# Performance work log

Measured on AMD Instinct MI355X. Metric: run time of the kernel, lower is better.

Reference implementation:

```python
import jax, jax.numpy as jnp
import numpy as np

B, C, L, D, H = 8, 64, 128, 768, 768  # batch, candidates, tokens, hidden, mlp hidden


def setup_inputs() -> dict:
    key = jax.random.key(0)
    k0, k1, k2 = jax.random.split(key, 3)
    inp = jax.random.normal(k0, (B, C, 2, L, D), dtype=jnp.float32)
    # MlpModule params (input_size = 768*2): Linear(2D->H) -> ReLU -> Linear(H->1)
    W1 = jax.random.normal(k1, (2 * D, H), dtype=jnp.float32) * 0.02
    b1 = jnp.zeros((H,), dtype=jnp.float32)
    W2 = jax.random.normal(k2, (H, 1), dtype=jnp.float32) * 0.02
    b2 = jnp.zeros((1,), dtype=jnp.float32)
    return {"input": inp, "W1": W1, "b1": b1, "W2": W2, "b2": b2}


def reference(input, W1, b1, W2, b2):
    b, c, _, l, d = input.shape
    context = input[:, :, 0].reshape(b * c, l, d)  # [BC, L, D]
    entity = input[:, :, 1].reshape(b * c, l, d)   # [BC, L, D]
    mask = (context[:, :, 0] != 0).astype(context.dtype)  # [BC, L]

    # bmm similarity: [BC, L, L]
    sim = jnp.einsum('bld,bmd->blm', context, entity)
    dot_scores = jnp.max(sim, axis=-1)          # [BC, L]
    argmax_values = jnp.argmax(sim, axis=-1)    # [BC, L]

    # gather best-matching entity token per context token: [BC, L, D]
    gathered = jnp.take_along_axis(entity, argmax_values[..., None], axis=1)

    # MLP over stacked (context, entity) pair -> flatten to 2D features
    mlp_in = jnp.concatenate([context, gathered], axis=-1)  # [BC, L, 2D]
    h = jax.nn.relu(mlp_in @ W1 + b1)
    scores = (h @ W2 + b2)[..., 0]              # [BC, L]

    scores = jnp.sum(scores * mask, axis=-1)              # [BC]
    dot_scores = jnp.sum(dot_scores * mask, axis=-1).reshape(b, c)  # [B, C]
    return scores, dot_scores
```

## Files before the change

### kernel.cpp

```cpp
#include <hip/hip_runtime.h>
#include <hip/hip_bf16.h>
#include <stdint.h>

#define NPAIR 512
#define LTOK  128
#define DDIM  768
#define HDIM  768
#define K2    1536
#define MARGIN 0.4f

typedef float f32x4 __attribute__((ext_vector_type(4)));
typedef short bf16x8 __attribute__((ext_vector_type(8)));

static __device__ __forceinline__ int fsw(int row) {
    return (row ^ (row >> 2)) & 3;
}

static __device__ __forceinline__ unsigned short f2bf(float f) {
    union { float f; uint32_t u; } v; v.f = f;
    uint32_t u = v.u;
    u += 0x7FFF + ((u >> 16) & 1);
    return (unsigned short)(u >> 16);
}

static __device__ __forceinline__ uint2 pack4(f32x4 v) {
    __hip_bfloat162 lo = __float22bfloat162_rn(float2{v[0], v[1]});
    __hip_bfloat162 hi = __float22bfloat162_rn(float2{v[2], v[3]});
    uint2 r;
    r.x = *reinterpret_cast<unsigned*>(&lo);
    r.y = *reinterpret_cast<unsigned*>(&hi);
    return r;
}

static __device__ __forceinline__ uint4 pack8(f32x4 a, f32x4 b) {
    uint2 lo = pack4(a), hi = pack4(b);
    uint4 r; r.x = lo.x; r.y = lo.y; r.z = hi.x; r.w = hi.y;
    return r;
}

typedef const __attribute__((address_space(1))) void* gas_t;
typedef __attribute__((address_space(3))) void* las_t;
static __device__ __forceinline__ void gld16(const void* g, void* l) {
    __builtin_amdgcn_global_load_lds((gas_t)g, (las_t)l, 16, 0, 0);
}

static __device__ __forceinline__ float wave_dot(const float* __restrict__ a,
                                                 const float* __restrict__ b,
                                                 int lane) {
    f32x4 s4 = {0.f, 0.f, 0.f, 0.f};
#pragma unroll
    for (int it = 0; it < 3; ++it) {
        int k = it * 256 + lane * 4;
        f32x4 av = *(const f32x4*)(a + k);
        f32x4 bv = *(const f32x4*)(b + k);
#pragma unroll
        for (int q = 0; q < 4; ++q) s4[q] = fmaf(av[q], bv[q], s4[q]);
    }
    float v = (s4[0] + s4[1]) + (s4[2] + s4[3]);
#pragma unroll
    for (int m = 1; m < 64; m <<= 1) v += __shfl_xor(v, m);
    return v;
}

__global__ __launch_bounds__(512, 4) void simfma_kernel(
        const float* __restrict__ inp,
        float* __restrict__ dotmax, int* __restrict__ argmax,
        unsigned short* __restrict__ Cbf, unsigned short* __restrict__ Ebf)
{
    const int p    = blockIdx.x;
    const int t    = threadIdx.x;
    const int wv   = t >> 6;
    const int lane = t & 63;
    const int s    = lane & 15, g = lane >> 4;

    const float* Cbase = inp + (size_t)(2 * p) * LTOK * DDIM;
    const float* Ebase = Cbase + (size_t)LTOK * DDIM;

    __shared__ unsigned short Cl[2][128][32];
    __shared__ unsigned short El[2][128][32];
    __shared__ unsigned short cand[128][16];
    __shared__ int   ccnt[128];
    __shared__ float rm1[128];
    __shared__ int   ri1[128];

    if (t < 128) ccnt[t] = 0;

    f32x4 acc[8];
#pragma unroll
    for (int j = 0; j < 8; j++) acc[j] = (f32x4){0.f, 0.f, 0.f, 0.f};

    const int srow0 = t >> 3;
    const int srow1 = 64 + srow0;
    const int so8   = t & 7;
    const int sh    = so8 >> 2;
    const int sq    = so8 & 3;
    const int qs0   = (sq ^ fsw(srow0)) * 8;
    const int qs1   = (sq ^ fsw(srow1)) * 8;

    f32x4 cbuf[4], ebuf[4];

    auto ISSUE = [&](int kc) {
        const int k0 = kc * 64;
        const float* c0a = Cbase + (size_t)srow0 * DDIM + k0 + so8 * 8;
        const float* c1a = Cbase + (size_t)srow1 * DDIM + k0 + so8 * 8;
        const float* e0a = Ebase + (size_t)srow0 * DDIM + k0 + so8 * 8;
        const float* e1a = Ebase + (size_t)srow1 * DDIM + k0 + so8 * 8;
        cbuf[0] = *(const f32x4*)c0a;  cbuf[1] = *(const f32x4*)(c0a + 4);
        cbuf[2] = *(const f32x4*)c1a;  cbuf[3] = *(const f32x4*)(c1a + 4);
        ebuf[0] = *(const f32x4*)e0a;  ebuf[1] = *(const f32x4*)(e0a + 4);
        ebuf[2] = *(const f32x4*)e1a;  ebuf[3] = *(const f32x4*)(e1a + 4);
    };

    ISSUE(0);
    for (int kc = 0; kc < 12; ++kc) {
        const int k0 = kc * 64;
        uint4 cw0 = pack8(cbuf[0], cbuf[1]);
        uint4 cw1 = pack8(cbuf[2], cbuf[3]);
        uint4 ew0 = pack8(ebuf[0], ebuf[1]);
        uint4 ew1 = pack8(ebuf[2], ebuf[3]);
        *(uint4*)&Cl[sh][srow0][qs0] = cw0;
        *(uint4*)&Cl[sh][srow1][qs1] = cw1;
        *(uint4*)&El[sh][srow0][qs0] = ew0;
        *(uint4*)&El[sh][srow1][qs1] = ew1;
        __syncthreads();

        if (kc < 11) ISSUE(kc + 1);
        {
            size_t o0 = ((size_t)p * LTOK + srow0) * DDIM + k0 + so8 * 8;
            size_t o1 = ((size_t)p * LTOK + srow1) * DDIM + k0 + so8 * 8;
            *(uint4*)(Cbf + o0) = cw0;
            *(uint4*)(Cbf + o1) = cw1;
            *(uint4*)(Ebf + o0) = ew0;
            *(uint4*)(Ebf + o1) = ew1;
        }

#pragma unroll
        for (int h = 0; h < 2; ++h) {
            const int arow = wv * 16 + s;
            bf16x8 af = *(const bf16x8*)&Cl[h][arow][(g ^ fsw(arow)) * 8];
            bf16x8 bfr[8];
#pragma unroll
            for (int j = 0; j < 8; ++j) {
                const int row = j * 16 + s;
                bfr[j] = *(const bf16x8*)&El[h][row][(g ^ fsw(row)) * 8];
            }
#pragma unroll
            for (int j = 0; j < 8; ++j)
                acc[j] = __builtin_amdgcn_mfma_f32_16x16x32_bf16(af, bfr[j], acc[j], 0, 0, 0);
        }
        __syncthreads();
    }

#pragma unroll
    for (int r = 0; r < 4; ++r) {
        float m1 = acc[0][r]; int i1 = s; float m2 = -1e30f;
#pragma unroll
        for (int j = 1; j < 8; ++j) {
            float v = acc[j][r]; int c = j * 16 + s;
            if (v > m1 || (v == m1 && c < i1)) { m2 = m1; m1 = v; i1 = c; }
            else if (v > m2) m2 = v;
        }
#pragma unroll
        for (int msk = 1; msk < 16; msk <<= 1) {
            float o1 = __shfl_xor(m1, msk);
            int   oi = __shfl_xor(i1, msk);
            float o2 = __shfl_xor(m2, msk);
            bool take = (o1 > m1) || (o1 == m1 && oi < i1);
            float nm2 = take ? fmaxf(m1, o2) : fmaxf(m2, o1);
            if (take) { m1 = o1; i1 = oi; }
            m2 = nm2;
        }
        int row = wv * 16 + g * 4 + r;
        if (s == 0) { rm1[row] = m1; ri1[row] = i1; }
        float thr = m1 - MARGIN;
#pragma unroll
        for (int j = 0; j < 8; ++j) {
            float v = acc[j][r]; int c = j * 16 + s;
            if (v >= thr && c != i1) {
                int idx = atomicAdd(&ccnt[row], 1);
                if (idx < 16) cand[row][idx] = (unsigned short)c;
            }
        }
    }
    __syncthreads();

    for (int rr = 0; rr < 16; ++rr) {
        int row = wv + rr * 8;
        int cnt = ccnt[row];
        float m1 = rm1[row]; int i1 = ri1[row];
        size_t ob = (size_t)p * LTOK + row;
        if (cnt == 0) {
            if (lane == 0) { dotmax[ob] = m1; argmax[ob] = i1; }
            continue;
        }
        const float* cr = Cbase + (size_t)row * DDIM;
        float bv; int bc;
        if (cnt <= 16) {
            bv = wave_dot(cr, Ebase + (size_t)i1 * DDIM, lane); bc = i1;
            for (int q = 0; q < cnt; ++q) {
                int c = cand[row][q];
                float v = wave_dot(cr, Ebase + (size_t)c * DDIM, lane);
                if (v > bv || (v == bv && c < bc)) { bv = v; bc = c; }
            }
        } else {
            bv = -1e30f; bc = 0;
            for (int c = 0; c < 128; ++c) {
                float v = wave_dot(cr, Ebase + (size_t)c * DDIM, lane);
                if (v > bv || (v == bv && c < bc)) { bv = v; bc = c; }
            }
        }
        if (lane == 0) { dotmax[ob] = bv; argmax[ob] = bc; }
    }
}

__global__ __launch_bounds__(256) void w1t_kernel(
        const float* __restrict__ W1, unsigned short* __restrict__ W1T)
{
    int idx = blockIdx.x * 256 + threadIdx.x;
    if (idx >= HDIM * K2 / 8) return;
    int c  = idx / (K2 / 8);
    int k0 = (idx % (K2 / 8)) * 8;
    unsigned short v[8];
#pragma unroll
    for (int q = 0; q < 8; q++) v[q] = f2bf(W1[(size_t)(k0 + q) * HDIM + c]);
    *(uint4*)(W1T + (size_t)c * K2 + k0) = *(const uint4*)v;
}

__global__ __launch_bounds__(256, 2) void mlp2_kernel(
        const unsigned short* __restrict__ Cbf,
        const unsigned short* __restrict__ Ebf,
        const unsigned short* __restrict__ W1T,
        const float* __restrict__ b1,
        const float* __restrict__ W2,
        const int* __restrict__ argmax,
        float* __restrict__ part)
{
    const int p    = blockIdx.x;
    const int cbk  = blockIdx.y;
    const int t    = threadIdx.x;
    const int wv   = t >> 6;
    const int lane = t & 63;
    const int s    = lane & 15, g = lane >> 4;
    const int wr   = wv >> 1, wc = wv & 1;

    __shared__ unsigned short Ald[2][128][32];
    __shared__ unsigned short Bld[2][256][32];
    __shared__ int am[128];

    if (t < 128) am[t] = argmax[p * LTOK + t];

    f32x4 acc[4][8];
#pragma unroll
    for (int i = 0; i < 4; i++)
#pragma unroll
        for (int j = 0; j < 8; j++) acc[i][j] = (f32x4){0.f, 0.f, 0.f, 0.f};

    const int rsub = lane >> 2;
    const int chk  = lane & 3;

    auto STAGE = [&](int buf, int kt) {
        const int k0   = kt * 32;
        const bool ctx = (kt < 24);
        const int kloc = ctx ? k0 : (k0 - DDIM);
#pragma unroll
        for (int n = 0; n < 4; ++n) {
            int c0  = (wv * 4 + n) * 16;
            int col = c0 + rsub;
            int ck  = chk ^ fsw(col);
            gld16(W1T + (size_t)(cbk * 256 + col) * K2 + k0 + ck * 8,
                  &Bld[buf][c0][0]);
        }
#pragma unroll
        for (int n = 0; n < 2; ++n) {
            int r0 = (wv * 2 + n) * 16;
            int r  = r0 + rsub;
            int ck = chk ^ fsw(r);
            const unsigned short* base = ctx
                ? (Cbf + ((size_t)p * LTOK + r) * DDIM)
                : (Ebf + ((size_t)p * LTOK + am[r]) * DDIM);
            gld16(base + kloc + ck * 8, &Ald[buf][r0][0]);
        }
    };

    STAGE(0, 0);
    __syncthreads();

    int cur = 0;
    for (int kt = 0; kt < 47; ++kt) {
        STAGE(cur ^ 1, kt + 1);
        bf16x8 af[4], bfr[8];
#pragma unroll
        for (int i = 0; i < 4; ++i) {
            const int row = wr * 64 + i * 16 + s;
            af[i] = *(const bf16x8*)&Ald[cur][row][(g ^ fsw(row)) * 8];
        }
#pragma unroll
        for (int j = 0; j < 8; ++j) {
            const int row = wc * 128 + j * 16 + s;
            bfr[j] = *(const bf16x8*)&Bld[cur][row][(g ^ fsw(row)) * 8];
        }
#pragma unroll
        for (int i = 0; i < 4; ++i)
#pragma unroll
            for (int j = 0; j < 8; ++j)
                acc[i][j] = __builtin_amdgcn_mfma_f32_16x16x32_bf16(af[i], bfr[j], acc[i][j], 0, 0, 0);
        __syncthreads();
        cur ^= 1;
    }
    {
        bf16x8 af[4], bfr[8];
#pragma unroll
        for (int i = 0; i < 4; ++i) {
            const int row = wr * 64 + i * 16 + s;
            af[i] = *(const bf16x8*)&Ald[cur][row][(g ^ fsw(row)) * 8];
        }
#pragma unroll
        for (int j = 0; j < 8; ++j) {
            const int row = wc * 128 + j * 16 + s;
            bfr[j] = *(const bf16x8*)&Bld[cur][row][(g ^ fsw(row)) * 8];
        }
#pragma unroll
        for (int i = 0; i < 4; ++i)
#pragma unroll
            for (int j = 0; j < 8; ++j)
                acc[i][j] = __builtin_amdgcn_mfma_f32_16x16x32_bf16(af[i], bfr[j], acc[i][j], 0, 0, 0);
    }

    float w2v[8], b1v[8];
#pragma unroll
    for (int j = 0; j < 8; j++) {
        int col = cbk * 256 + wc * 128 + j * 16 + s;
        w2v[j] = W2[col];
        b1v[j] = b1[col];
    }
    float ssum[4][4];
#pragma unroll
    for (int i = 0; i < 4; i++)
#pragma unroll
        for (int r = 0; r < 4; r++) ssum[i][r] = 0.f;
#pragma unroll
    for (int i = 0; i < 4; i++)
#pragma unroll
        for (int j = 0; j < 8; j++)
#pragma unroll
            for (int r = 0; r < 4; r++) {
                float h = acc[i][j][r] + b1v[j];
                h = h > 0.f ? h : 0.f;
                ssum[i][r] = fmaf(h, w2v[j], ssum[i][r]);
            }
#pragma unroll
    for (int sft = 1; sft < 16; sft <<= 1)
#pragma unroll
        for (int i = 0; i < 4; i++)
#pragma unroll
            for (int r = 0; r < 4; r++) ssum[i][r] += __shfl_xor(ssum[i][r], sft);
    if (s == 0) {
        const int q = cbk * 2 + wc;
#pragma unroll
        for (int i = 0; i < 4; i++)
#pragma unroll
            for (int r = 0; r < 4; r++)
                part[(size_t)q * (NPAIR * LTOK) + p * LTOK + wr * 64 + i * 16 + g * 4 + r]
                    = ssum[i][r];
    }
}

__global__ __launch_bounds__(128) void reduce6_kernel(
        const float* __restrict__ inp,
        const float* __restrict__ part,
        const float* __restrict__ dotmax,
        const float* __restrict__ b2,
        float* __restrict__ out)
{
    int p = blockIdx.x;
    int l = threadIdx.x;
    float c0  = inp[((size_t)(2 * p) * LTOK + l) * DDIM];
    float msk = (c0 != 0.0f) ? 1.f : 0.f;
    float sc = b2[0];
#pragma unroll
    for (int q = 0; q < 6; ++q)
        sc += part[(size_t)q * (NPAIR * LTOK) + p * LTOK + l];
    sc *= msk;
    float dm = dotmax[p * LTOK + l] * msk;
#pragma unroll
    for (int sh = 1; sh < 64; sh <<= 1) {
        sc += __shfl_xor(sc, sh);
        dm += __shfl_xor(dm, sh);
    }
    __shared__ float tmp[4];
    if ((l & 63) == 0) { tmp[(l >> 6) * 2] = sc; tmp[(l >> 6) * 2 + 1] = dm; }
    __syncthreads();
    if (l == 0) {
        out[p]          = tmp[0] + tmp[2];
        out[NPAIR + p]  = tmp[1] + tmp[3];
    }
}

__global__ __launch_bounds__(256) void sim_fp32_kernel(
        const float* __restrict__ inp,
        float* __restrict__ dotmax, int* __restrict__ argmax)
{
    const int p  = blockIdx.x;
    const int t  = threadIdx.x;
    const int tx = t & 15, ty = t >> 4;
    const float* Cbase = inp + (size_t)(2 * p) * LTOK * DDIM;
    const float* Ebase = Cbase + (size_t)LTOK * DDIM;

    __shared__ float Ct[128][36];
    __shared__ float Et[128][36];

    float acc[8][8];
#pragma unroll
    for (int i = 0; i < 8; i++)
#pragma unroll
        for (int j = 0; j < 8; j++) acc[i][j] = 0.f;

    for (int kc = 0; kc < 24; ++kc) {
        const int k0 = kc * 32;
#pragma unroll
        for (int q = 0; q < 4; ++q) {
            int f = q * 256 + t;
            int row = f >> 3, c4 = f & 7;
            *(f32x4*)&Ct[row][c4 * 4] = *(const f32x4*)(Cbase + (size_t)row * DDIM + k0 + c4 * 4);
            *(f32x4*)&Et[row][c4 * 4] = *(const f32x4*)(Ebase + (size_t)row * DDIM + k0 + c4 * 4);
        }
        __syncthreads();
#pragma unroll
        for (int kk4 = 0; kk4 < 8; ++kk4) {
            f32x4 cr[8], er[8];
#pragma unroll
            for (int i = 0; i < 8; i++) cr[i] = *(const f32x4*)&Ct[ty + 16 * i][kk4 * 4];
#pragma unroll
            for (int j = 0; j < 8; j++) er[j] = *(const f32x4*)&Et[tx + 16 * j][kk4 * 4];
#pragma unroll
            for (int kk = 0; kk < 4; kk++)
#pragma unroll
                for (int i = 0; i < 8; i++)
#pragma unroll
                    for (int j = 0; j < 8; j++)
                        acc[i][j] = fmaf(cr[i][kk], er[j][kk], acc[i][j]);
        }
        __syncthreads();
    }
#pragma unroll
    for (int i = 0; i < 8; i++) {
        float m = acc[i][0]; int mi = tx;
#pragma unroll
        for (int j = 1; j < 8; j++) {
            int c = tx + 16 * j;
            float v = acc[i][j];
            if (v > m || (v == m && c < mi)) { m = v; mi = c; }
        }
#pragma unroll
        for (int sft = 1; sft < 16; sft <<= 1) {
            float vo = __shfl_xor(m, sft);
            int   io = __shfl_xor(mi, sft);
            if (vo > m || (vo == m && io < mi)) { m = vo; mi = io; }
        }
        if (tx == 0) {
            int r = ty + 16 * i;
            dotmax[(size_t)p * LTOK + r] = m;
            argmax[(size_t)p * LTOK + r] = mi;
        }
    }
}

__global__ __launch_bounds__(256, 2) void mlp_kernel(
        const float* __restrict__ inp,
        const unsigned short* __restrict__ W1T,
        const float* __restrict__ b1,
        const float* __restrict__ W2,
        const int* __restrict__ argmax,
        float* __restrict__ tokscore)
{
    const int tile = blockIdx.x;
    const int cb   = blockIdx.y;
    const int t    = threadIdx.x;
    const int wv   = t >> 6;
    const int lane = t & 63;
    const int s    = lane & 15, g = lane >> 4;

    __shared__ unsigned short At[64][32];
    __shared__ unsigned short Bt[384][32];
    __shared__ int am[64];

    if (t < 64) am[t] = argmax[tile * 64 + t];
    __syncthreads();

    f32x4 acc[4][6];
#pragma unroll
    for (int i = 0; i < 4; i++)
#pragma unroll
        for (int j = 0; j < 6; j++) acc[i][j] = (f32x4){0.f, 0.f, 0.f, 0.f};

    for (int kc = 0; kc < 48; ++kc) {
        const int k0  = kc * 32;
        const int sel = (kc >= 24) ? 1 : 0;
        const int kloc = k0 - sel * DDIM;
#pragma unroll
        for (int q = 0; q < 2; ++q) {
            int f = q * 256 + t;
            int row = f >> 3, c4 = f & 7;
            int token = tile * 64 + row;
            int pp = token >> 7;
            int lsel = sel ? am[row] : (token & 127);
            const float* src = inp + ((size_t)(2 * pp + sel) * LTOK + lsel) * DDIM + kloc + c4 * 4;
            f32x4 v = *(const f32x4*)src;
            uint2 pk = pack4(v);
            *(uint2*)&At[row][c4 * 4] = pk;
        }
#pragma unroll
        for (int q = 0; q < 6; ++q) {
            int f = q * 256 + t;
            int colr = f >> 2, q8 = f & 3;
            const unsigned short* src = W1T + (size_t)(cb * 384 + colr) * K2 + k0 + q8 * 8;
            *(uint4*)&Bt[colr][q8 * 8] = *(const uint4*)src;
        }
        __syncthreads();

        bf16x8 af[4], bfr[6];
#pragma unroll
        for (int i = 0; i < 4; i++) af[i]  = *(const bf16x8*)&At[i * 16 + s][g * 8];
#pragma unroll
        for (int j = 0; j < 6; j++) bfr[j] = *(const bf16x8*)&Bt[wv * 96 + j * 16 + s][g * 8];
#pragma unroll
        for (int i = 0; i < 4; i++)
#pragma unroll
            for (int j = 0; j < 6; j++)
                acc[i][j] = __builtin_amdgcn_mfma_f32_16x16x32_bf16(af[i], bfr[j], acc[i][j], 0, 0, 0);
        __syncthreads();
    }

    float w2v[6], b1v[6];
#pragma unroll
    for (int j = 0; j < 6; j++) {
        int col = cb * 384 + wv * 96 + j * 16 + s;
        w2v[j] = W2[col];
        b1v[j] = b1[col];
    }
    float ssum[4][4];
#pragma unroll
    for (int i = 0; i < 4; i++)
#pragma unroll
        for (int r = 0; r < 4; r++) ssum[i][r] = 0.f;
#pragma unroll
    for (int i = 0; i < 4; i++)
#pragma unroll
        for (int j = 0; j < 6; j++)
#pragma unroll
            for (int r = 0; r < 4; r++) {
                float h = acc[i][j][r] + b1v[j];
                h = h > 0.f ? h : 0.f;
                ssum[i][r] = fmaf(h, w2v[j], ssum[i][r]);
            }
#pragma unroll
    for (int sft = 1; sft < 16; sft <<= 1)
#pragma unroll
        for (int i = 0; i < 4; i++)
#pragma unroll
            for (int r = 0; r < 4; r++) ssum[i][r] += __shfl_xor(ssum[i][r], sft);
    if (s == 0) {
#pragma unroll
        for (int i = 0; i < 4; i++)
#pragma unroll
            for (int r = 0; r < 4; r++)
                atomicAdd(&tokscore[tile * 64 + i * 16 + g * 4 + r], ssum[i][r]);
    }
}

__global__ __launch_bounds__(128) void reduce_kernel(
        const float* __restrict__ inp,
        const float* __restrict__ tokscore,
        const float* __restrict__ dotmax,
        const float* __restrict__ b2,
        float* __restrict__ out)
{
    int p = blockIdx.x;
    int l = threadIdx.x;
    float c0  = inp[((size_t)(2 * p) * LTOK + l) * DDIM];
    float msk = (c0 != 0.0f) ? 1.f : 0.f;
    float sc  = (tokscore[p * LTOK + l] + b2[0]) * msk;
    float dm  = dotmax[p * LTOK + l] * msk;
#pragma unroll
    for (int sh = 1; sh < 64; sh <<= 1) {
        sc += __shfl_xor(sc, sh);
        dm += __shfl_xor(dm, sh);
    }
    __shared__ float tmp[4];
    if ((l & 63) == 0) { tmp[(l >> 6) * 2] = sc; tmp[(l >> 6) * 2 + 1] = dm; }
    __syncthreads();
    if (l == 0) {
        out[p]          = tmp[0] + tmp[2];
        out[NPAIR + p]  = tmp[1] + tmp[3];
    }
}

extern "C" void kernel_launch(void* const* d_in, const int* in_sizes, int n_in,
                              void* d_out, int out_size, void* d_ws, size_t ws_size,
                              hipStream_t stream)
{
    const float* inp = (const float*)d_in[0];
    const float* W1  = (const float*)d_in[1];
    const float* b1  = (const float*)d_in[2];
    const float* W2  = (const float*)d_in[3];
    const float* b2  = (const float*)d_in[4];
    float* out = (float*)d_out;

    char* ws = (char*)d_ws;
    unsigned short* W1T   = (unsigned short*)ws;
    float*          dotmx = (float*)(ws + 2359296);
    int*            amax  = (int*)(ws + 2359296 + 262144);
    float*          toksc = (float*)(ws + 2359296 + 2*262144);
    unsigned short* Cbf   = (unsigned short*)(ws + 2359296 + 3*262144);
    unsigned short* Ebf   = Cbf + (size_t)NPAIR * LTOK * DDIM;
    float*          part  = (float*)(ws + 2359296 + 3*262144 + 2*100663296ull);
    const size_t NEED = 2359296ull + 3ull*262144ull + 2ull*100663296ull + 6ull*262144ull;

    const bool big = ws_size >= NEED;

    w1t_kernel<<<(HDIM * K2 / 8 + 255) / 256, 256, 0, stream>>>(W1, W1T);
    if (big) {
        simfma_kernel<<<NPAIR, 512, 0, stream>>>(inp, dotmx, amax, Cbf, Ebf);
        mlp2_kernel<<<dim3(NPAIR, 3), 256, 0, stream>>>(Cbf, Ebf, W1T, b1, W2, amax, part);
        reduce6_kernel<<<NPAIR, 128, 0, stream>>>(inp, part, dotmx, b2, out);
    } else {
        hipMemsetAsync(toksc, 0, 65536 * sizeof(float), stream);
        sim_fp32_kernel<<<NPAIR, 256, 0, stream>>>(inp, dotmx, amax);
        mlp_kernel<<<dim3(1024, 2), 256, 0, stream>>>(inp, W1T, b1, W2, amax, toksc);
        reduce_kernel<<<NPAIR, 128, 0, stream>>>(inp, toksc, dotmx, b2, out);
    }
}
```

Before: 324.2 us.

## Fuse similarity, MLP and final reduction into one per-pair kernel

Merges the similarity/argmax kernel, the MLP GEMM kernel and the reduction kernel into a single kernel with one block per pair. argmax, dotmax and per-token scores stay in shared memory, the three H column blocks are looped inside the block, and the token sum and mask are applied in-block. This removes two launches and the global round-trips for argmax, dotmax and the partial scores. In exchange, grid parallelism for the MLP drops from 1536 blocks to 512, W1T is re-streamed by each block, and the bf16 C/E copies are still written and then re-read inside the same kernel.

```diff
diff --git a/kernel.cpp b/kernel.cpp
--- a/kernel.cpp
+++ b/kernel.cpp
@@ -62,10 +62,14 @@
     return v;
 }
 
-__global__ __launch_bounds__(512, 4) void simfma_kernel(
+__global__ __launch_bounds__(512, 4) void fused_kernel(
         const float* __restrict__ inp,
-        float* __restrict__ dotmax, int* __restrict__ argmax,
-        unsigned short* __restrict__ Cbf, unsigned short* __restrict__ Ebf)
+        const unsigned short* __restrict__ W1T,
+        const float* __restrict__ b1,
+        const float* __restrict__ W2,
+        const float* __restrict__ b2,
+        unsigned short* __restrict__ Cbf, unsigned short* __restrict__ Ebf,
+        float* __restrict__ out)
 {
     const int p    = blockIdx.x;
     const int t    = threadIdx.x;
@@ -76,18 +80,23 @@
     const float* Cbase = inp + (size_t)(2 * p) * LTOK * DDIM;
     const float* Ebase = Cbase + (size_t)LTOK * DDIM;
 
-    __shared__ unsigned short Cl[2][128][32];
-    __shared__ unsigned short El[2][128][32];
-    __shared__ unsigned short cand[128][16];
-    __shared__ int   ccnt[128];
-    __shared__ float rm1[128];
-    __shared__ int   ri1[128];
-
-    if (t < 128) ccnt[t] = 0;
-
-    f32x4 acc[8];
-#pragma unroll
-    for (int j = 0; j < 8; j++) acc[j] = (f32x4){0.f, 0.f, 0.f, 0.f};
+    __shared__ char  pool[49152];
+    __shared__ int   am[128];
+    __shared__ float dm[128];
+    __shared__ float tok[128];
+
+    unsigned short (*Cl)[128][32] = (unsigned short (*)[128][32])pool;
+    unsigned short (*El)[128][32] = (unsigned short (*)[128][32])(pool + 16384);
+    unsigned short (*cand)[16]    = (unsigned short (*)[16])(pool + 32768);
+    int*   ccnt = (int*)(pool + 36864);
+    float* rm1  = (float*)(pool + 37376);
+    int*   ri1  = (int*)(pool + 37888);
+
+    if (t < 128) { ccnt[t] = 0; tok[t] = 0.f; }
+
+    f32x4 acc1[8];
+#pragma unroll
+    for (int j = 0; j < 8; j++) acc1[j] = (f32x4){0.f, 0.f, 0.f, 0.f};
 
     const int srow0 = t >> 3;
     const int srow1 = 64 + srow0;
@@ -146,17 +155,17 @@
             }
 #pragma unroll
             for (int j = 0; j < 8; ++j)
-                acc[j] = __builtin_amdgcn_mfma_f32_16x16x32_bf16(af, bfr[j], acc[j], 0, 0, 0);
+                acc1[j] = __builtin_amdgcn_mfma_f32_16x16x32_bf16(af, bfr[j], acc1[j], 0, 0, 0);
         }
         __syncthreads();
     }
 
 #pragma unroll
     for (int r = 0; r < 4; ++r) {
-        float m1 = acc[0][r]; int i1 = s; float m2 = -1e30f;
+        float m1 = acc1[0][r]; int i1 = s; float m2 = -1e30f;
 #pragma unroll
         for (int j = 1; j < 8; ++j) {
-            float v = acc[j][r]; int c = j * 16 + s;
+            float v = acc1[j][r]; int c = j * 16 + s;
             if (v > m1 || (v == m1 && c < i1)) { m2 = m1; m1 = v; i1 = c; }
             else if (v > m2) m2 = v;
         }
@@ -175,7 +184,7 @@
         float thr = m1 - MARGIN;
 #pragma unroll
         for (int j = 0; j < 8; ++j) {
-            float v = acc[j][r]; int c = j * 16 + s;
+            float v = acc1[j][r]; int c = j * 16 + s;
             if (v >= thr && c != i1) {
                 int idx = atomicAdd(&ccnt[row], 1);
                 if (idx < 16) cand[row][idx] = (unsigned short)c;
@@ -188,9 +197,8 @@
         int row = wv + rr * 8;
         int cnt = ccnt[row];
         float m1 = rm1[row]; int i1 = ri1[row];
-        size_t ob = (size_t)p * LTOK + row;
         if (cnt == 0) {
-            if (lane == 0) { dotmax[ob] = m1; argmax[ob] = i1; }
+            if (lane == 0) { dm[row] = m1; am[row] = i1; }
             continue;
         }
         const float* cr = Cbase + (size_t)row * DDIM;
@@ -209,7 +217,127 @@
                 if (v > bv || (v == bv && c < bc)) { bv = v; bc = c; }
             }
         }
-        if (lane == 0) { dotmax[ob] = bv; argmax[ob] = bc; }
+        if (lane == 0) { dm[row] = bv; am[row] = bc; }
+    }
+    __syncthreads();
+
+    unsigned short (*Ald)[128][32] = (unsigned short (*)[128][32])pool;
+    unsigned short (*Bld)[256][32] = (unsigned short (*)[256][32])(pool + 16384);
+
+    const int wr  = wv >> 2, wcg = wv & 3;
+    const int rsub = lane >> 2;
+    const int chk  = lane & 3;
+
+    for (int cb = 0; cb < 3; ++cb) {
+        f32x4 acc[4][4];
+#pragma unroll
+        for (int i = 0; i < 4; i++)
+#pragma unroll
+            for (int j = 0; j < 4; j++) acc[i][j] = (f32x4){0.f, 0.f, 0.f, 0.f};
+
+        auto STAGE = [&](int buf, int kt) {
+            const int k0   = kt * 32;
+            const bool ctx = (kt < 24);
+            const int kloc = ctx ? k0 : (k0 - DDIM);
+#pragma unroll
+            for (int n = 0; n < 2; ++n) {
+                int r0  = (wv * 2 + n) * 16;
+                int col = r0 + rsub;
+                int ck  = chk ^ fsw(col);
+                gld16(W1T + (size_t)(cb * 256 + col) * K2 + k0 + ck * 8,
+                      &Bld[buf][r0][0]);
+            }
+            {
+                int r0 = wv * 16;
+                int r  = r0 + rsub;
+                int ck = chk ^ fsw(r);
+                const unsigned short* base = ctx
+                    ? (Cbf + ((size_t)p * LTOK + r) * DDIM)
+                    : (Ebf + ((size_t)p * LTOK + am[r]) * DDIM);
+                gld16(base + kloc + ck * 8, &Ald[buf][r0][0]);
+            }
+        };
+
+        STAGE(0, 0);
+        __syncthreads();
+        int cur = 0;
+        for (int kt = 0; kt < 48; ++kt) {
+            if (kt < 47) STAGE(cur ^ 1, kt + 1);
+            bf16x8 af[4], bfr[4];
+#pragma unroll
+            for (int i = 0; i < 4; ++i) {
+                const int row = wr * 64 + i * 16 + s;
+                af[i] = *(const bf16x8*)&Ald[cur][row][(g ^ fsw(row)) * 8];
+            }
+#pragma unroll
+            for (int j = 0; j < 4; ++j) {
+                const int brow = wcg * 64 + j * 16 + s;
+                bfr[j] = *(const bf16x8*)&Bld[cur][brow][(g ^ fsw(brow)) * 8];
+            }
+#pragma unroll
+            for (int i = 0; i < 4; ++i)
+#pragma unroll
+                for (int j = 0; j < 4; ++j)
+                    acc[i][j] = __builtin_amdgcn_mfma_f32_16x16x32_bf16(af[i], bfr[j], acc[i][j], 0, 0, 0);
+            __syncthreads();
+            cur ^= 1;
+        }
+
+        float w2v[4], b1v[4];
+#pragma unroll
+        for (int j = 0; j < 4; j++) {
+            int col = cb * 256 + wcg * 64 + j * 16 + s;
+            w2v[j] = W2[col];
+            b1v[j] = b1[col];
+        }
+        float ss[4][4];
+#pragma unroll
+        for (int i = 0; i < 4; i++)
+#pragma unroll
+            for (int r = 0; r < 4; r++) ss[i][r] = 0.f;
+#pragma unroll
+        for (int i = 0; i < 4; i++)
+#pragma unroll
+            for (int j = 0; j < 4; j++)
+#pragma unroll
+                for (int r = 0; r < 4; r++) {
+                    float h = acc[i][j][r] + b1v[j];
+                    h = h > 0.f ? h : 0.f;
+                    ss[i][r] = fmaf(h, w2v[j], ss[i][r]);
+                }
+#pragma unroll
+        for (int sft = 1; sft < 16; sft <<= 1)
+#pragma unroll
+            for (int i = 0; i < 4; i++)
+#pragma unroll
+                for (int r = 0; r < 4; r++) ss[i][r] += __shfl_xor(ss[i][r], sft);
+        if (s == 0) {
+#pragma unroll
+            for (int i = 0; i < 4; i++)
+#pragma unroll
+                for (int r = 0; r < 4; r++)
+                    atomicAdd(&tok[wr * 64 + i * 16 + g * 4 + r], ss[i][r]);
+        }
+    }
+    __syncthreads();
+
+    if (wv == 0) {
+        float b2v = b2[0];
+        float sc = 0.f, dd = 0.f;
+#pragma unroll
+        for (int rr = 0; rr < 2; ++rr) {
+            int row = lane + rr * 64;
+            float c0 = Cbase[(size_t)row * DDIM];
+            float mk = (c0 != 0.f) ? 1.f : 0.f;
+            sc += mk * (tok[row] + b2v);
+            dd += mk * dm[row];
+        }
+#pragma unroll
+        for (int m = 1; m < 64; m <<= 1) {
+            sc += __shfl_xor(sc, m);
+            dd += __shfl_xor(dd, m);
+        }
+        if (lane == 0) { out[p] = sc; out[NPAIR + p] = dd; }
     }
 }
 
@@ -224,176 +352,6 @@
 #pragma unroll
     for (int q = 0; q < 8; q++) v[q] = f2bf(W1[(size_t)(k0 + q) * HDIM + c]);
     *(uint4*)(W1T + (size_t)c * K2 + k0) = *(const uint4*)v;
-}
-
-__global__ __launch_bounds__(256, 2) void mlp2_kernel(
-        const unsigned short* __restrict__ Cbf,
-        const unsigned short* __restrict__ Ebf,
-        const unsigned short* __restrict__ W1T,
-        const float* __restrict__ b1,
-        const float* __restrict__ W2,
-        const int* __restrict__ argmax,
-        float* __restrict__ part)
-{
-    const int p    = blockIdx.x;
-    const int cbk  = blockIdx.y;
-    const int t    = threadIdx.x;
-    const int wv   = t >> 6;
-    const int lane = t & 63;
-    const int s    = lane & 15, g = lane >> 4;
-    const int wr   = wv >> 1, wc = wv & 1;
-
-    __shared__ unsigned short Ald[2][128][32];
-    __shared__ unsigned short Bld[2][256][32];
-    __shared__ int am[128];
-
-    if (t < 128) am[t] = argmax[p * LTOK + t];
-
-    f32x4 acc[4][8];
-#pragma unroll
-    for (int i = 0; i < 4; i++)
-#pragma unroll
-        for (int j = 0; j < 8; j++) acc[i][j] = (f32x4){0.f, 0.f, 0.f, 0.f};
-
-    const int rsub = lane >> 2;
-    const int chk  = lane & 3;
-
-    auto STAGE = [&](int buf, int kt) {
-        const int k0   = kt * 32;
-        const bool ctx = (kt < 24);
-        const int kloc = ctx ? k0 : (k0 - DDIM);
-#pragma unroll
-        for (int n = 0; n < 4; ++n) {
-            int c0  = (wv * 4 + n) * 16;
-            int col = c0 + rsub;
-            int ck  = chk ^ fsw(col);
-            gld16(W1T + (size_t)(cbk * 256 + col) * K2 + k0 + ck * 8,
-                  &Bld[buf][c0][0]);
-        }
-#pragma unroll
-        for (int n = 0; n < 2; ++n) {
-            int r0 = (wv * 2 + n) * 16;
-            int r  = r0 + rsub;
-            int ck = chk ^ fsw(r);
-            const unsigned short* base = ctx
-                ? (Cbf + ((size_t)p * LTOK + r) * DDIM)
-                : (Ebf + ((size_t)p * LTOK + am[r]) * DDIM);
-            gld16(base + kloc + ck * 8, &Ald[buf][r0][0]);
-        }
-    };
-
-    STAGE(0, 0);
-    __syncthreads();
-
-    int cur = 0;
-    for (int kt = 0; kt < 47; ++kt) {
-        STAGE(cur ^ 1, kt + 1);
-        bf16x8 af[4], bfr[8];
-#pragma unroll
-        for (int i = 0; i < 4; ++i) {
-            const int row = wr * 64 + i * 16 + s;
-            af[i] = *(const bf16x8*)&Ald[cur][row][(g ^ fsw(row)) * 8];
-        }
-#pragma unroll
-        for (int j = 0; j < 8; ++j) {
-            const int row = wc * 128 + j * 16 + s;
-            bfr[j] = *(const bf16x8*)&Bld[cur][row][(g ^ fsw(row)) * 8];
-        }
-#pragma unroll
-        for (int i = 0; i < 4; ++i)
-#pragma unroll
-            for (int j = 0; j < 8; ++j)
-                acc[i][j] = __builtin_amdgcn_mfma_f32_16x16x32_bf16(af[i], bfr[j], acc[i][j], 0, 0, 0);
-        __syncthreads();
-        cur ^= 1;
-    }
-    {
-        bf16x8 af[4], bfr[8];
-#pragma unroll
-        for (int i = 0; i < 4; ++i) {
-            const int row = wr * 64 + i * 16 + s;
-            af[i] = *(const bf16x8*)&Ald[cur][row][(g ^ fsw(row)) * 8];
-        }
-#pragma unroll
-        for (int j = 0; j < 8; ++j) {
-            const int row = wc * 128 + j * 16 + s;
-            bfr[j] = *(const bf16x8*)&Bld[cur][row][(g ^ fsw(row)) * 8];
-        }
-#pragma unroll
-        for (int i = 0; i < 4; ++i)
-#pragma unroll
-            for (int j = 0; j < 8; ++j)
-                acc[i][j] = __builtin_amdgcn_mfma_f32_16x16x32_bf16(af[i], bfr[j], acc[i][j], 0, 0, 0);
-    }
-
-    float w2v[8], b1v[8];
-#pragma unroll
-    for (int j = 0; j < 8; j++) {
-        int col = cbk * 256 + wc * 128 + j * 16 + s;
-        w2v[j] = W2[col];
-        b1v[j] = b1[col];
-    }
-    float ssum[4][4];
-#pragma unroll
-    for (int i = 0; i < 4; i++)
-#pragma unroll
-        for (int r = 0; r < 4; r++) ssum[i][r] = 0.f;
-#pragma unroll
-    for (int i = 0; i < 4; i++)
-#pragma unroll
-        for (int j = 0; j < 8; j++)
-#pragma unroll
-            for (int r = 0; r < 4; r++) {
-                float h = acc[i][j][r] + b1v[j];
-                h = h > 0.f ? h : 0.f;
-                ssum[i][r] = fmaf(h, w2v[j], ssum[i][r]);
-            }
-#pragma unroll
-    for (int sft = 1; sft < 16; sft <<= 1)
-#pragma unroll
-        for (int i = 0; i < 4; i++)
-#pragma unroll
-            for (int r = 0; r < 4; r++) ssum[i][r] += __shfl_xor(ssum[i][r], sft);
-    if (s == 0) {
-        const int q = cbk * 2 + wc;
-#pragma unroll
-        for (int i = 0; i < 4; i++)
-#pragma unroll
-            for (int r = 0; r < 4; r++)
-                part[(size_t)q * (NPAIR * LTOK) + p * LTOK + wr * 64 + i * 16 + g * 4 + r]
-                    = ssum[i][r];
-    }
-}
-
-__global__ __launch_bounds__(128) void reduce6_kernel(
-        const float* __restrict__ inp,
-        const float* __restrict__ part,
-        const float* __restrict__ dotmax,
-        const float* __restrict__ b2,
-        float* __restrict__ out)
-{
-    int p = blockIdx.x;
-    int l = threadIdx.x;
-    float c0  = inp[((size_t)(2 * p) * LTOK + l) * DDIM];
-    float msk = (c0 != 0.0f) ? 1.f : 0.f;
-    float sc = b2[0];
-#pragma unroll
-    for (int q = 0; q < 6; ++q)
-        sc += part[(size_t)q * (NPAIR * LTOK) + p * LTOK + l];
-    sc *= msk;
-    float dm = dotmax[p * LTOK + l] * msk;
-#pragma unroll
-    for (int sh = 1; sh < 64; sh <<= 1) {
-        sc += __shfl_xor(sc, sh);
-        dm += __shfl_xor(dm, sh);
-    }
-    __shared__ float tmp[4];
-    if ((l & 63) == 0) { tmp[(l >> 6) * 2] = sc; tmp[(l >> 6) * 2 + 1] = dm; }
-    __syncthreads();
-    if (l == 0) {
-        out[p]          = tmp[0] + tmp[2];
-        out[NPAIR + p]  = tmp[1] + tmp[3];
-    }
 }
 
 __global__ __launch_bounds__(256) void sim_fp32_kernel(
@@ -613,16 +571,13 @@
     float*          toksc = (float*)(ws + 2359296 + 2*262144);
     unsigned short* Cbf   = (unsigned short*)(ws + 2359296 + 3*262144);
     unsigned short* Ebf   = Cbf + (size_t)NPAIR * LTOK * DDIM;
-    float*          part  = (float*)(ws + 2359296 + 3*262144 + 2*100663296ull);
-    const size_t NEED = 2359296ull + 3ull*262144ull + 2ull*100663296ull + 6ull*262144ull;
+    const size_t NEED = 2359296ull + 3ull*262144ull + 2ull*100663296ull;
 
     const bool big = ws_size >= NEED;
 
     w1t_kernel<<<(HDIM * K2 / 8 + 255) / 256, 256, 0, stream>>>(W1, W1T);
     if (big) {
-        simfma_kernel<<<NPAIR, 512, 0, stream>>>(inp, dotmx, amax, Cbf, Ebf);
-        mlp2_kernel<<<dim3(NPAIR, 3), 256, 0, stream>>>(Cbf, Ebf, W1T, b1, W2, amax, part);
-        reduce6_kernel<<<NPAIR, 128, 0, stream>>>(inp, part, dotmx, b2, out);
+        fused_kernel<<<NPAIR, 512, 0, stream>>>(inp, W1T, b1, W2, b2, Cbf, Ebf, out);
     } else {
         hipMemsetAsync(toksc, 0, 65536 * sizeof(float), stream);
         sim_fp32_kernel<<<NPAIR, 256, 0, stream>>>(inp, dotmx, amax);
```

New measurement: 303.8 us. 6.3% less time.
